# Kernel tuning notes

Hardware: AMD Instinct MI355X
Metric: run time of the kernel (lower is better)

## Reference

```python
import jax, jax.numpy as jnp
import numpy as np

# SelectiveAttention (keras) reference.
# - A single shared InputDense (D -> key_dim) projects query, key, value.
# - ComponentBuilder yields (filter_input=Q, context_input=banded K^T, _input=V):
#   scores = (Q K^T / sqrt(key_dim)) masked to the band |i-j| <= band_size
#   (the layer's Softmax sublayer is built but never invoked in call()).
# - attended = scores @ V, then OutputDense (key_dim -> D). Dropout inactive at inference.

def setup_inputs() -> dict:
    key = jax.random.key(0)
    ks = jax.random.split(key, 5)
    B, S, D, Dk = 4, 4096, 512, 64
    query = jax.random.normal(ks[0], (B, S, D), dtype=jnp.float32)
    value = jax.random.normal(ks[1], (B, S, D), dtype=jnp.float32)
    Wi = jax.random.normal(ks[2], (D, Dk), dtype=jnp.float32) * (1.0 / np.sqrt(D))
    bi = jnp.zeros((Dk,), dtype=jnp.float32)
    Wo = jax.random.normal(ks[3], (Dk, D), dtype=jnp.float32) * (1.0 / np.sqrt(Dk))
    bo = jnp.zeros((D,), dtype=jnp.float32)
    return {"query": query, "value": value, "Wi": Wi, "bi": bi,
            "Wo": Wo, "bo": bo, "band_size": 128}


def reference(query, value, Wi, bi, Wo, bo, band_size):
    Dk = Wi.shape[1]
    scale = 1.0 / jnp.sqrt(jnp.asarray(Dk, dtype=query.dtype))
    # shared input projection (same dense for q, k, v; key defaults to value)
    q = query @ Wi + bi            # [B,S,Dk]
    kv = value @ Wi + bi           # [B,S,Dk]  (k == v here)
    scores = jnp.einsum('bqd,bkd->bqk', q, kv) * scale  # [B,S,S]
    S = q.shape[1]
    idx = jnp.arange(S)
    band = (jnp.abs(idx[:, None] - idx[None, :]) <= band_size)  # [S,S] bool
    scores = jnp.where(band[None], scores, 0.0)
    attended = jnp.einsum('bqk,bkd->bqd', scores, kv)    # [B,S,Dk]
    return attended @ Wo + bo                            # [B,S,D]
```

## Files before the change

### kernel.cpp

```cpp
#include <hip/hip_runtime.h>
#include <math.h>


typedef __bf16 bf16;
using bf16x4  = __attribute__((ext_vector_type(4))) __bf16;
using bf16x8  = __attribute__((ext_vector_type(8))) __bf16;
using floatx4 = __attribute__((ext_vector_type(4))) float;

#define MFMA(a, b, c) __builtin_amdgcn_mfma_f32_16x16x32_bf16(a, b, c, 0, 0, 0)

__global__ __launch_bounds__(256) void prep_weights(
    const float* __restrict__ Wi, const float* __restrict__ Wo,
    bf16* __restrict__ WiT, bf16* __restrict__ WoT)
{
    __shared__ float T[64][65];
    const int blk = blockIdx.x, tid = threadIdx.x;
    if (blk < 8) {
        const int k0 = blk * 64;
        #pragma unroll
        for (int i = 0; i < 4; i++) {
            int idx4 = tid * 4 + i;
            int r = idx4 >> 4, c4 = (idx4 & 15) * 4;
            float4 f = *(const float4*)(Wi + (size_t)(k0 + r) * 64 + c4);
            T[r][c4 + 0] = f.x; T[r][c4 + 1] = f.y;
            T[r][c4 + 2] = f.z; T[r][c4 + 3] = f.w;
        }
        __syncthreads();
        #pragma unroll
        for (int i = 0; i < 2; i++) {
            int seg = tid * 2 + i;
            int n = seg >> 3, k8 = (seg & 7) * 8;
            bf16x8 v;
            #pragma unroll
            for (int j = 0; j < 8; j++) v[j] = (bf16)T[k8 + j][n];
            *(bf16x8*)(WiT + (size_t)n * 512 + k0 + k8) = v;
        }
    } else {
        const int n0 = (blk - 8) * 64;
        #pragma unroll
        for (int i = 0; i < 4; i++) {
            int idx4 = tid * 4 + i;
            int r = idx4 >> 4, c4 = (idx4 & 15) * 4;
            float4 f = *(const float4*)(Wo + (size_t)r * 512 + n0 + c4);
            T[r][c4 + 0] = f.x; T[r][c4 + 1] = f.y;
            T[r][c4 + 2] = f.z; T[r][c4 + 3] = f.w;
        }
        __syncthreads();
        #pragma unroll
        for (int i = 0; i < 2; i++) {
            int seg = tid * 2 + i;
            int n = seg >> 3, k8 = (seg & 7) * 8;
            bf16x8 v;
            #pragma unroll
            for (int j = 0; j < 8; j++) v[j] = (bf16)T[k8 + j][n];
            *(bf16x8*)(WoT + (size_t)(n0 + n) * 64 + k8) = v;
        }
    }
}

__global__ __launch_bounds__(256, 4) void proj_in_kernel(
    const float* __restrict__ v, const bf16* __restrict__ WiT,
    const float* __restrict__ bi, bf16* __restrict__ kvp,
    bf16* __restrict__ kvT, int K, int S)
{
    __shared__ float P[4][16][68];
    const int tid = threadIdx.x;
    const int wave = tid >> 6, lane = tid & 63;
    const int lr = lane & 15, lq = lane >> 4;
    const int row0 = blockIdx.x * 16;
    const float* xrow = v + (size_t)(row0 + lr) * K + wave * 128;
    const bf16* wrow = WiT + wave * 128;

    floatx4 acc[4] = {};
    #pragma unroll
    for (int ks = 0; ks < 4; ks++) {
        const int k0 = ks * 32 + lq * 8;
        float4 a0 = *(const float4*)(xrow + k0);
        float4 a1 = *(const float4*)(xrow + k0 + 4);
        bf16x8 af;
        af[0] = (bf16)a0.x; af[1] = (bf16)a0.y; af[2] = (bf16)a0.z; af[3] = (bf16)a0.w;
        af[4] = (bf16)a1.x; af[5] = (bf16)a1.y; af[6] = (bf16)a1.z; af[7] = (bf16)a1.w;
        #pragma unroll
        for (int t = 0; t < 4; t++) {
            bf16x8 bfv = *(const bf16x8*)(wrow + (size_t)(t * 16 + lr) * K + k0);
            acc[t] = MFMA(af, bfv, acc[t]);
        }
    }
    #pragma unroll
    for (int t = 0; t < 4; t++)
        #pragma unroll
        for (int r = 0; r < 4; r++)
            P[wave][lq * 4 + r][t * 16 + lr] = acc[t][r];
    __syncthreads();

    {
        const int row = tid >> 4, c4 = (tid & 15) * 4;
        float4 s0 = *(const float4*)&P[0][row][c4];
        float4 s1 = *(const float4*)&P[1][row][c4];
        float4 s2 = *(const float4*)&P[2][row][c4];
        float4 s3 = *(const float4*)&P[3][row][c4];
        float4 bb = *(const float4*)(bi + c4);
        bf16x4 o;
        o[0] = (bf16)(s0.x + s1.x + s2.x + s3.x + bb.x);
        o[1] = (bf16)(s0.y + s1.y + s2.y + s3.y + bb.y);
        o[2] = (bf16)(s0.z + s1.z + s2.z + s3.z + bb.z);
        o[3] = (bf16)(s0.w + s1.w + s2.w + s3.w + bb.w);
        *(bf16x4*)(kvp + (size_t)(row0 + row) * 64 + c4) = o;
    }
    {
        const int d = tid >> 2, s4 = (tid & 3) * 4;
        const int b = row0 >> 12, s0r = row0 & (S - 1);
        const float bb = bi[d];
        bf16x4 o;
        #pragma unroll
        for (int i = 0; i < 4; i++) {
            float s = P[0][s4 + i][d] + P[1][s4 + i][d]
                    + P[2][s4 + i][d] + P[3][s4 + i][d] + bb;
            o[i] = (bf16)s;
        }
        *(bf16x4*)(kvT + ((size_t)b * 64 + d) * S + s0r + s4) = o;
    }
}

__global__ __launch_bounds__(64, 2) void band_attn_out_kernel(
    const float* __restrict__ query, const bf16* __restrict__ WiT,
    const float* __restrict__ bi, const bf16* __restrict__ kvp,
    const bf16* __restrict__ kvT, const int* __restrict__ band_ptr,
    const bf16* __restrict__ WoT, const float* __restrict__ bo,
    float* __restrict__ out, int K, int S, float scale)
{
    __shared__ bf16 Qs[16][80];
    __shared__ bf16 Ss[16][336];
    const int lane = threadIdx.x;
    const int lr = lane & 15, lq = lane >> 4;
    const int gs = blockIdx.x;
    const int b = gs >> 8;
    const int q0 = (gs & 255) * 16;
    const int band = band_ptr[0];

    {
        const float* xrow = query + ((size_t)b * S + q0 + lr) * K;
        floatx4 qa[4] = {};
        #pragma unroll
        for (int ks = 0; ks < 16; ks++) {
            const int k0 = ks * 32 + lq * 8;
            float4 a0 = *(const float4*)(xrow + k0);
            float4 a1 = *(const float4*)(xrow + k0 + 4);
            bf16x8 af;
            af[0] = (bf16)a0.x; af[1] = (bf16)a0.y; af[2] = (bf16)a0.z; af[3] = (bf16)a0.w;
            af[4] = (bf16)a1.x; af[5] = (bf16)a1.y; af[6] = (bf16)a1.z; af[7] = (bf16)a1.w;
            #pragma unroll
            for (int t = 0; t < 4; t++) {
                bf16x8 bfv = *(const bf16x8*)(WiT + (size_t)(t * 16 + lr) * K + k0);
                qa[t] = MFMA(af, bfv, qa[t]);
            }
        }
        #pragma unroll
        for (int t = 0; t < 4; t++) {
            float bb = bi[t * 16 + lr];
            #pragma unroll
            for (int r = 0; r < 4; r++)
                Qs[lq * 4 + r][t * 16 + lr] = (bf16)((qa[t][r] + bb) * scale);
        }
    }
    bf16x8 qf0 = *(const bf16x8*)(&Qs[lr][lq * 8]);
    bf16x8 qf1 = *(const bf16x8*)(&Qs[lr][32 + lq * 8]);

    const int base = ((q0 - band) >> 6) * 64;
    #pragma unroll
    for (int h = 0; h < 10; h++) {
        const int kj0 = base + h * 32;
        floatx4 sc[2] = {};
        #pragma unroll
        for (int t2 = 0; t2 < 2; t2++) {
            int kr = kj0 + t2 * 16 + lr;
            int krc = min(max(kr, 0), S - 1);
            const bf16* kp = kvp + ((size_t)b * S + krc) * 64;
            bf16x8 b0 = *(const bf16x8*)(kp + lq * 8);
            bf16x8 b1 = *(const bf16x8*)(kp + 32 + lq * 8);
            sc[t2] = MFMA(qf0, b0, sc[t2]);
            sc[t2] = MFMA(qf1, b1, sc[t2]);
        }
        const int lo = kj0, hi = kj0 + 31;
        const bool full = (lo >= 0) && (hi < S) &&
                          (lo >= q0 + 15 - band) && (hi <= q0 + band);
        if (full) {
            #pragma unroll
            for (int t2 = 0; t2 < 2; t2++)
                #pragma unroll
                for (int r = 0; r < 4; r++)
                    Ss[lq * 4 + r][h * 32 + t2 * 16 + lr] = (bf16)sc[t2][r];
        } else {
            #pragma unroll
            for (int t2 = 0; t2 < 2; t2++) {
                int kj = kj0 + t2 * 16 + lr;
                bool kv_ok = (kj >= 0) && (kj < S);
                #pragma unroll
                for (int r = 0; r < 4; r++) {
                    int qi = q0 + lq * 4 + r;
                    int dlt = qi - kj; dlt = dlt < 0 ? -dlt : dlt;
                    float vv = (kv_ok && dlt <= band) ? sc[t2][r] : 0.f;
                    Ss[lq * 4 + r][h * 32 + t2 * 16 + lr] = (bf16)vv;
                }
            }
        }
    }

    floatx4 acc[4] = {};
    #pragma unroll
    for (int h = 0; h < 10; h++) {
        bf16x8 sa = *(const bf16x8*)(&Ss[lr][h * 32 + lq * 8]);
        int kb = base + h * 32 + lq * 8;
        int kbc = min(max(kb, 0), S - 8);
        #pragma unroll
        for (int t = 0; t < 4; t++) {
            bf16x8 vb = *(const bf16x8*)(kvT + ((size_t)b * 64 + t * 16 + lr) * S + kbc);
            acc[t] = MFMA(sa, vb, acc[t]);
        }
    }
    #pragma unroll
    for (int t = 0; t < 4; t++)
        #pragma unroll
        for (int r = 0; r < 4; r++)
            Qs[lq * 4 + r][t * 16 + lr] = (bf16)acc[t][r];
    bf16x8 af0 = *(const bf16x8*)(&Qs[lr][lq * 8]);
    bf16x8 af1 = *(const bf16x8*)(&Qs[lr][32 + lq * 8]);

    float* orow = out + ((size_t)b * S + q0) * 512;
    #pragma unroll
    for (int tp = 0; tp < 32; tp++) {
        const bf16* wp = WoT + (size_t)(tp * 16 + lr) * 64;
        bf16x8 w0 = *(const bf16x8*)(wp + lq * 8);
        bf16x8 w1 = *(const bf16x8*)(wp + 32 + lq * 8);
        floatx4 o = {};
        o = MFMA(w0, af0, o);
        o = MFMA(w1, af1, o);
        float4 bb = *(const float4*)(bo + tp * 16 + lq * 4);
        float4 ov;
        ov.x = o[0] + bb.x; ov.y = o[1] + bb.y;
        ov.z = o[2] + bb.z; ov.w = o[3] + bb.w;
        *(float4*)(orow + (size_t)lr * 512 + tp * 16 + lq * 4) = ov;
    }
}

extern "C" void kernel_launch(void* const* d_in, const int* in_sizes, int n_in,
                              void* d_out, int out_size, void* d_ws, size_t ws_size,
                              hipStream_t stream) {
    const float* query = (const float*)d_in[0];
    const float* value = (const float*)d_in[1];
    const float* Wi    = (const float*)d_in[2];
    const float* bi    = (const float*)d_in[3];
    const float* Wo    = (const float*)d_in[4];
    const float* bo    = (const float*)d_in[5];
    const int*   band  = (const int*)d_in[6];
    float* out = (float*)d_out;

    const int Dk = in_sizes[3];
    const int D  = in_sizes[5];
    const int S  = 4096;
    const int BS = in_sizes[0] / D;
    const int B  = BS / S;
    const float scale = 1.0f / sqrtf((float)Dk);

    bf16* WiT = (bf16*)d_ws;
    bf16* WoT = WiT + 32768;
    bf16* kvp = WoT + 32768;
    bf16* kvT = kvp + (size_t)BS * 64;

    prep_weights<<<16, 256, 0, stream>>>(Wi, Wo, WiT, WoT);

    proj_in_kernel<<<dim3(BS / 16), 256, 0, stream>>>(
        value, WiT, bi, kvp, kvT, D, S);

    band_attn_out_kernel<<<dim3(BS / 16), 64, 0, stream>>>(
        query, WiT, bi, kvp, kvT, band, WoT, bo, out, D, S, scale);
}
```

Measured before the change: 145.1 us.

## Move query projection into the 256-thread projection kernel alongside value projection

The query projection (D->Dk GEMM with bias and scale) moves out of the single-wave band attention kernel and into the projection kernel, which now launches twice as many blocks and dispatches on block index to handle either query or value rows. The projected, scaled Q is written to a new bf16 workspace buffer, and the attention kernel loads its Q fragments directly from it. This spreads the K-dimension work across four waves instead of one 64-thread block, removing a long serial prologue from the attention kernel. The cost is an extra global write and read of the Q tensor and more workspace memory.

```diff
diff --git a/kernel.cpp b/kernel.cpp
--- a/kernel.cpp
+++ b/kernel.cpp
@@ -58,17 +58,21 @@
     }
 }
 
-__global__ __launch_bounds__(256, 4) void proj_in_kernel(
-    const float* __restrict__ v, const bf16* __restrict__ WiT,
-    const float* __restrict__ bi, bf16* __restrict__ kvp,
-    bf16* __restrict__ kvT, int K, int S)
+__global__ __launch_bounds__(256, 4) void proj_kernel(
+    const float* __restrict__ query, const float* __restrict__ value,
+    const bf16* __restrict__ WiT, const float* __restrict__ bi,
+    bf16* __restrict__ kvp, bf16* __restrict__ kvT, bf16* __restrict__ qp,
+    int K, int S, float scale, int NBV)
 {
     __shared__ float P[4][16][68];
     const int tid = threadIdx.x;
     const int wave = tid >> 6, lane = tid & 63;
     const int lr = lane & 15, lq = lane >> 4;
-    const int row0 = blockIdx.x * 16;
-    const float* xrow = v + (size_t)(row0 + lr) * K + wave * 128;
+    const bool isQ = (int)blockIdx.x >= NBV;
+    const int blk = isQ ? ((int)blockIdx.x - NBV) : (int)blockIdx.x;
+    const int row0 = blk * 16;
+    const float* src = isQ ? query : value;
+    const float* xrow = src + (size_t)(row0 + lr) * K + wave * 128;
     const bf16* wrow = WiT + wave * 128;
 
     floatx4 acc[4] = {};
@@ -100,14 +104,16 @@
         float4 s2 = *(const float4*)&P[2][row][c4];
         float4 s3 = *(const float4*)&P[3][row][c4];
         float4 bb = *(const float4*)(bi + c4);
+        const float m = isQ ? scale : 1.0f;
+        bf16* dst = isQ ? qp : kvp;
         bf16x4 o;
-        o[0] = (bf16)(s0.x + s1.x + s2.x + s3.x + bb.x);
-        o[1] = (bf16)(s0.y + s1.y + s2.y + s3.y + bb.y);
-        o[2] = (bf16)(s0.z + s1.z + s2.z + s3.z + bb.z);
-        o[3] = (bf16)(s0.w + s1.w + s2.w + s3.w + bb.w);
-        *(bf16x4*)(kvp + (size_t)(row0 + row) * 64 + c4) = o;
-    }
-    {
+        o[0] = (bf16)((s0.x + s1.x + s2.x + s3.x + bb.x) * m);
+        o[1] = (bf16)((s0.y + s1.y + s2.y + s3.y + bb.y) * m);
+        o[2] = (bf16)((s0.z + s1.z + s2.z + s3.z + bb.z) * m);
+        o[3] = (bf16)((s0.w + s1.w + s2.w + s3.w + bb.w) * m);
+        *(bf16x4*)(dst + (size_t)(row0 + row) * 64 + c4) = o;
+    }
+    if (!isQ) {
         const int d = tid >> 2, s4 = (tid & 3) * 4;
         const int b = row0 >> 12, s0r = row0 & (S - 1);
         const float bb = bi[d];
@@ -123,11 +129,10 @@
 }
 
 __global__ __launch_bounds__(64, 2) void band_attn_out_kernel(
-    const float* __restrict__ query, const bf16* __restrict__ WiT,
-    const float* __restrict__ bi, const bf16* __restrict__ kvp,
+    const bf16* __restrict__ qp, const bf16* __restrict__ kvp,
     const bf16* __restrict__ kvT, const int* __restrict__ band_ptr,
     const bf16* __restrict__ WoT, const float* __restrict__ bo,
-    float* __restrict__ out, int K, int S, float scale)
+    float* __restrict__ out, int S)
 {
     __shared__ bf16 Qs[16][80];
     __shared__ bf16 Ss[16][336];
@@ -138,33 +143,9 @@
     const int q0 = (gs & 255) * 16;
     const int band = band_ptr[0];
 
-    {
-        const float* xrow = query + ((size_t)b * S + q0 + lr) * K;
-        floatx4 qa[4] = {};
-        #pragma unroll
-        for (int ks = 0; ks < 16; ks++) {
-            const int k0 = ks * 32 + lq * 8;
-            float4 a0 = *(const float4*)(xrow + k0);
-            float4 a1 = *(const float4*)(xrow + k0 + 4);
-            bf16x8 af;
-            af[0] = (bf16)a0.x; af[1] = (bf16)a0.y; af[2] = (bf16)a0.z; af[3] = (bf16)a0.w;
-            af[4] = (bf16)a1.x; af[5] = (bf16)a1.y; af[6] = (bf16)a1.z; af[7] = (bf16)a1.w;
-            #pragma unroll
-            for (int t = 0; t < 4; t++) {
-                bf16x8 bfv = *(const bf16x8*)(WiT + (size_t)(t * 16 + lr) * K + k0);
-                qa[t] = MFMA(af, bfv, qa[t]);
-            }
-        }
-        #pragma unroll
-        for (int t = 0; t < 4; t++) {
-            float bb = bi[t * 16 + lr];
-            #pragma unroll
-            for (int r = 0; r < 4; r++)
-                Qs[lq * 4 + r][t * 16 + lr] = (bf16)((qa[t][r] + bb) * scale);
-        }
-    }
-    bf16x8 qf0 = *(const bf16x8*)(&Qs[lr][lq * 8]);
-    bf16x8 qf1 = *(const bf16x8*)(&Qs[lr][32 + lq * 8]);
+    const bf16* qrow = qp + ((size_t)b * S + q0 + lr) * 64;
+    bf16x8 qf0 = *(const bf16x8*)(qrow + lq * 8);
+    bf16x8 qf1 = *(const bf16x8*)(qrow + 32 + lq * 8);
 
     const int base = ((q0 - band) >> 6) * 64;
     #pragma unroll
@@ -266,12 +247,15 @@
     bf16* WoT = WiT + 32768;
     bf16* kvp = WoT + 32768;
     bf16* kvT = kvp + (size_t)BS * 64;
+    bf16* qp  = kvT + (size_t)BS * 64;
+
+    const int NBV = BS / 16;
 
     prep_weights<<<16, 256, 0, stream>>>(Wi, Wo, WiT, WoT);
 
-    proj_in_kernel<<<dim3(BS / 16), 256, 0, stream>>>(
-        value, WiT, bi, kvp, kvT, D, S);
-
-    band_attn_out_kernel<<<dim3(BS / 16), 64, 0, stream>>>(
-        query, WiT, bi, kvp, kvT, band, WoT, bo, out, D, S, scale);
-}
+    proj_kernel<<<dim3(2 * NBV), 256, 0, stream>>>(
+        query, value, WiT, bi, kvp, kvT, qp, D, S, scale, NBV);
+
+    band_attn_out_kernel<<<dim3(NBV), 64, 0, stream>>>(
+        qp, kvp, kvT, band, WoT, bo, out, S);
+}
```

Result: slower. 150.8 us (+3.9%).
